# Kernel tuning notes

Hardware: AMD Instinct MI355X
Metric: run time of the kernel (lower is better)

## Reference

```python
import jax, jax.numpy as jnp
import numpy as np

N = 100000   # nodes
E = 1250000  # edges per graph
D = 64       # in_feats
H = 64       # hidden_dim
C = 129      # num_classes
EPS = 1e-5


def setup_inputs() -> dict:
    key = jax.random.key(0)
    ks = jax.random.split(key, 32)
    nrm = lambda k, s: jax.random.normal(k, s, jnp.float32) * 0.05
    inp = {
        'node_features': jax.random.normal(ks[0], (N, D), jnp.float32),
        'm_src': jax.random.randint(ks[1], (E,), 0, N, jnp.int32),
        'm_dst': jax.random.randint(ks[2], (E,), 0, N, jnp.int32),
        'r_src': jax.random.randint(ks[3], (E,), 0, N, jnp.int32),
        'r_dst': jax.random.randint(ks[4], (E,), 0, N, jnp.int32),
    }
    i = 5
    for pre in ('soc', 'rt'):
        inp[pre + '_W1'] = nrm(ks[i], (D, H)); inp[pre + '_b1'] = jnp.zeros((H,), jnp.float32)
        inp[pre + '_g1'] = jnp.ones((H,), jnp.float32); inp[pre + '_bt1'] = jnp.zeros((H,), jnp.float32)
        inp[pre + '_W2'] = nrm(ks[i + 1], (H, H)); inp[pre + '_b2'] = jnp.zeros((H,), jnp.float32)
        inp[pre + '_g2'] = jnp.ones((H,), jnp.float32); inp[pre + '_bt2'] = jnp.zeros((H,), jnp.float32)
        i += 2
    inp['gW1'] = nrm(ks[i], (4 * H, H)); inp['gb1'] = jnp.zeros((H,), jnp.float32)
    inp['prelu_a'] = jnp.full((1,), 0.25, jnp.float32)
    inp['gW2'] = nrm(ks[i + 1], (H, H)); inp['gb2'] = jnp.zeros((H,), jnp.float32)
    inp['fcW'] = nrm(ks[i + 2], (H, C)); inp['fcb'] = jnp.zeros((C,), jnp.float32)
    return inp


def _gconv(h, src, dst, W, b):
    # DGL GraphConv, norm='both': D_out^{-1/2} (scatter-sum) D_in^{-1/2}, linear, ELU
    ones = jnp.ones(src.shape[0], jnp.float32)
    deg_o = jax.ops.segment_sum(ones, src, num_segments=N)
    deg_i = jax.ops.segment_sum(ones, dst, num_segments=N)
    ns = jax.lax.rsqrt(jnp.clip(deg_o, 1.0))
    nd = jax.lax.rsqrt(jnp.clip(deg_i, 1.0))
    agg = jax.ops.segment_sum((h * ns[:, None])[src], dst, num_segments=N)
    return jax.nn.elu((agg * nd[:, None]) @ W + b)


def _bn(x, g, b):
    mu = x.mean(0)
    v = x.var(0)
    return (x - mu) * jax.lax.rsqrt(v + EPS) * g + b


def _branch(x, src, dst, W1, b1, g1, bt1, W2, b2, g2, bt2):
    h = _bn(_gconv(x, src, dst, W1, b1), g1, bt1)
    return _bn(_gconv(h, src, dst, W2, b2), g2, bt2)


def reference(node_features, m_src, m_dst, r_src, r_dst,
              soc_W1, soc_b1, soc_g1, soc_bt1, soc_W2, soc_b2, soc_g2, soc_bt2,
              rt_W1, rt_b1, rt_g1, rt_bt1, rt_W2, rt_b2, rt_g2, rt_bt2,
              gW1, gb1, prelu_a, gW2, gb2, fcW, fcb):
    h1 = _branch(node_features, m_src, m_dst, soc_W1, soc_b1, soc_g1, soc_bt1, soc_W2, soc_b2, soc_g2, soc_bt2)
    h2 = _branch(node_features, r_src, r_dst, rt_W1, rt_b1, rt_g1, rt_bt1, rt_W2, rt_b2, rt_g2, rt_bt2)
    cat = jnp.concatenate([h1, h2, jnp.abs(h1 - h2), h1 * h2], axis=-1)
    z = cat @ gW1 + gb1
    z = jnp.where(z > 0, z, prelu_a * z)  # PReLU (single shared slope)
    gate = jax.nn.sigmoid(z @ gW2 + gb2)
    fused = gate * h1 + (1.0 - gate) * h2
    return fused @ fcW + fcb
```

## Files before the change

### kernel.cpp

```cpp
#include <hip/hip_runtime.h>
#include <math.h>

#define NN 100000
#define NE 1250000
#define HD 64
#define NCLS 129
#define NTILES 6250
#define GRID_T 782

#define NCH 64
#define CHU ((NE + NCH - 1) / NCH)
#define SUBR 50000
#define NW2 12500
#define NHE2 ((NN + 1) * (size_t)HD)

typedef float f32x4 __attribute__((ext_vector_type(4)));
typedef short bf16x8 __attribute__((ext_vector_type(8)));

__device__ __forceinline__ short f2b(float f) {
    unsigned u = __builtin_bit_cast(unsigned, f);
    u += 0x7FFFu + ((u >> 16) & 1u);
    return (short)(u >> 16);
}
__device__ __forceinline__ float b2f(short s) {
    return __builtin_bit_cast(float, ((unsigned)(unsigned short)s) << 16);
}

__global__ __launch_bounds__(1024) void k_hist8(
    const int* __restrict__ d0, const int* __restrict__ s0,
    const int* __restrict__ d1, const int* __restrict__ s1,
    unsigned char* __restrict__ P8d, unsigned char* __restrict__ P8s) {
    __shared__ unsigned int hw[NW2];
    int b = blockIdx.x, s = blockIdx.y, z = blockIdx.z;
    int g = z >> 1, arr = z & 1;
    const int* __restrict__ idx = arr ? (g ? s1 : s0) : (g ? d1 : d0);
    for (int i = threadIdx.x; i < NW2; i += 1024) hw[i] = 0;
    __syncthreads();
    int lo = s * SUBR;
    int beg = b * CHU, end = beg + CHU;
    if (end > NE) end = NE;
    for (int i = beg + threadIdx.x; i < end; i += 1024) {
        int v = idx[i] - lo;
        if ((unsigned)v < (unsigned)SUBR)
            atomicAdd(&hw[v >> 2], 1u << ((v & 3) * 8));
    }
    __syncthreads();
    unsigned char* base = arr ? P8s : P8d;
    unsigned int* dst = (unsigned int*)(base + ((size_t)(g * NCH + b)) * NN + lo);
    for (int i = threadIdx.x; i < NW2; i += 1024) dst[i] = hw[i];
}

__global__ void k_reduce8(unsigned int* __restrict__ Pd, const unsigned int* __restrict__ Ps,
                          float* __restrict__ ns, float* __restrict__ nd,
                          int* __restrict__ degi) {
    int w = blockIdx.x * 256 + threadIdx.x;
    if (w >= NN / 4) return;
    int g = blockIdx.y;
    Pd += (size_t)g * NCH * (NN / 4);
    Ps += (size_t)g * NCH * (NN / 4);
    ns += (size_t)g * (NN + 1); nd += (size_t)g * NN; degi += (size_t)g * NN;
    if (w == 0) ns[NN] = 0.f;
    unsigned run = 0;
#pragma unroll 8
    for (int b = 0; b < NCH; ++b) {
        size_t o = (size_t)b * (NN / 4) + w;
        unsigned v = Pd[o];
        Pd[o] = run;
        run += v;
    }
    unsigned so = 0;
#pragma unroll 8
    for (int b = 0; b < NCH; ++b) so += Ps[(size_t)b * (NN / 4) + w];
#pragma unroll
    for (int j = 0; j < 4; ++j) {
        int din = (run >> (8 * j)) & 255;
        int dout = (so >> (8 * j)) & 255;
        int node = w * 4 + j;
        degi[node] = din;
        ns[node] = rsqrtf((float)(dout < 1 ? 1 : dout));
        nd[node] = rsqrtf((float)(din < 1 ? 1 : din));
    }
}

__global__ void k_scan_local(const int* __restrict__ deg, int* __restrict__ excl,
                             int* __restrict__ bsums) {
    __shared__ int sm[1024];
    int g = blockIdx.y;
    deg += (size_t)g * NN; excl += (size_t)g * (NN + 1); bsums += g * 1024;
    int t = threadIdx.x;
    int i = blockIdx.x * 1024 + t;
    int v = (i < NN) ? deg[i] : 0;
    sm[t] = v;
    __syncthreads();
    for (int ofs = 1; ofs < 1024; ofs <<= 1) {
        int x = (t >= ofs) ? sm[t - ofs] : 0;
        __syncthreads();
        sm[t] += x;
        __syncthreads();
    }
    if (i < NN) excl[i] = sm[t] - v;
    if (t == 1023) bsums[blockIdx.x] = sm[1023];
}

__global__ void k_scan_tops(int* __restrict__ bsums, int nb) {
    __shared__ int sm[1024];
    bsums += blockIdx.y * 1024;
    int t = threadIdx.x;
    int v = (t < nb) ? bsums[t] : 0;
    sm[t] = v;
    __syncthreads();
    for (int ofs = 1; ofs < 1024; ofs <<= 1) {
        int x = (t >= ofs) ? sm[t - ofs] : 0;
        __syncthreads();
        sm[t] += x;
        __syncthreads();
    }
    if (t < nb) bsums[t] = sm[t] - v;
}

__global__ void k_scan_add(int* __restrict__ excl, const int* __restrict__ bsums) {
    int g = blockIdx.y;
    excl += (size_t)g * (NN + 1); bsums += g * 1024;
    int i = blockIdx.x * blockDim.x + threadIdx.x;
    if (i < NN) excl[i] += bsums[i >> 10];
    if (i == 0) excl[NN] = NE;
}

__global__ __launch_bounds__(1024) void k_fill8(
    const int* __restrict__ d0, const int* __restrict__ d1,
    const int* __restrict__ s0, const int* __restrict__ s1,
    const int* __restrict__ rowptr, const unsigned char* __restrict__ Pofs,
    int* __restrict__ col) {
    __shared__ unsigned int cur[NW2];
    int b = blockIdx.x, s = blockIdx.y, g = blockIdx.z;
    const int* __restrict__ dst = g ? d1 : d0;
    const int* __restrict__ src = g ? s1 : s0;
    rowptr += (size_t)g * (NN + 1);
    col += (size_t)g * NE;
    const unsigned char* __restrict__ ofs = Pofs + ((size_t)(g * NCH + b)) * NN;
    for (int i = threadIdx.x; i < NW2; i += 1024) cur[i] = 0;
    __syncthreads();
    int lo = s * SUBR;
    int beg = b * CHU, end = beg + CHU;
    if (end > NE) end = NE;
    for (int i = beg + threadIdx.x; i < end; i += 1024) {
        int d = dst[i] - lo;
        if ((unsigned)d < (unsigned)SUBR) {
            unsigned old = atomicAdd(&cur[d >> 2], 1u << ((d & 3) * 8));
            int r = (old >> ((d & 3) * 8)) & 255;
            int node = d + lo;
            col[rowptr[node] + (int)ofs[node] + r] = src[i];
        }
    }
}

__global__ void k_scale_nf(const float* __restrict__ nf, short* __restrict__ T) {
    int i = blockIdx.x * blockDim.x + threadIdx.x;
    if (i >= (NN + 1) * 8) return;
    int node = i >> 3;
    short r[8];
    if (node == NN) {
#pragma unroll
        for (int j = 0; j < 8; ++j) r[j] = 0;
    } else {
        const float4* p = (const float4*)(nf + (size_t)i * 8);
        float4 a = p[0], b = p[1];
        r[0] = f2b(a.x); r[1] = f2b(a.y); r[2] = f2b(a.z); r[3] = f2b(a.w);
        r[4] = f2b(b.x); r[5] = f2b(b.y); r[6] = f2b(b.z); r[7] = f2b(b.w);
    }
    *(bf16x8*)(T + (size_t)i * 8) = *(bf16x8*)r;
}

template <int NS>
__global__ __launch_bounds__(256) void k_gather(
    const short* __restrict__ tab, size_t tabStride, const float* __restrict__ ns,
    const float* __restrict__ nd, const int* __restrict__ rowptr,
    const int* __restrict__ col, short* __restrict__ out) {
    int w = (blockIdx.x * 256 + threadIdx.x) >> 6;
    int lane = threadIdx.x & 63;
    if (w >= NN) return;
    int g = blockIdx.y;
    tab += (size_t)g * tabStride; nd += (size_t)g * NN;
    rowptr += (size_t)g * (NN + 1); col += (size_t)g * NE; out += (size_t)g * NHE2;
    const float* nsA = ns + (size_t)g * (NN + 1);
    int grp = lane >> 4;
    int sub = lane & 15;
    int beg = rowptr[w], end = rowptr[w + 1];
    float a0 = 0.f, a1 = 0.f, a2 = 0.f, a3 = 0.f;
    for (int e0 = beg; e0 < end; e0 += 64) {
        int cnt = end - e0; if (cnt > 64) cnt = 64;
        int myc = (lane < cnt) ? col[e0 + lane] : NN;
        float myns = 0.f;
        if (NS) myns = nsA[myc];
        for (int j = 0; j < cnt; j += 16) {
#pragma unroll
            for (int u = 0; u < 4; ++u) {
                int idx = j + u * 4 + grp;
                int c = __shfl(myc, idx, 64);
                uint2 v = *(const uint2*)(tab + (size_t)c * HD + sub * 4);
                float v0 = __builtin_bit_cast(float, v.x << 16);
                float v1 = __builtin_bit_cast(float, v.x & 0xffff0000u);
                float v2 = __builtin_bit_cast(float, v.y << 16);
                float v3 = __builtin_bit_cast(float, v.y & 0xffff0000u);
                if (NS) {
                    float nsc = __shfl(myns, idx, 64);
                    a0 = fmaf(nsc, v0, a0); a1 = fmaf(nsc, v1, a1);
                    a2 = fmaf(nsc, v2, a2); a3 = fmaf(nsc, v3, a3);
                } else {
                    a0 += v0; a1 += v1; a2 += v2; a3 += v3;
                }
            }
        }
    }
    a0 += __shfl_xor(a0, 16, 64); a1 += __shfl_xor(a1, 16, 64);
    a2 += __shfl_xor(a2, 16, 64); a3 += __shfl_xor(a3, 16, 64);
    a0 += __shfl_xor(a0, 32, 64); a1 += __shfl_xor(a1, 32, 64);
    a2 += __shfl_xor(a2, 32, 64); a3 += __shfl_xor(a3, 32, 64);
    if (grp == 0) {
        float s = nd[w];
        unsigned r0 = ((unsigned)(unsigned short)f2b(a0 * s)) |
                      (((unsigned)(unsigned short)f2b(a1 * s)) << 16);
        unsigned r1 = ((unsigned)(unsigned short)f2b(a2 * s)) |
                      (((unsigned)(unsigned short)f2b(a3 * s)) << 16);
        uint2 r; r.x = r0; r.y = r1;
        *(uint2*)(out + (size_t)w * HD + sub * 4) = r;
    }
}

__global__ __launch_bounds__(256) void k_lin(
    const short* __restrict__ X, const float* __restrict__ Wa, const float* __restrict__ Wb,
    const float* __restrict__ ba, const float* __restrict__ bb,
    short* __restrict__ Y, float* __restrict__ stats) {
    __shared__ short sW[4096];
    __shared__ float sm2[128];
    int g = blockIdx.y;
    const float* W = g ? Wb : Wa;
    const float* bias = g ? bb : ba;
    X += (size_t)g * NHE2; Y += (size_t)g * NHE2; stats += (size_t)g * 128;
    int t = threadIdx.x;
    for (int i = t; i < 4096; i += 256) {
        int j = i & 7, l16i = (i >> 3) & 15, kgi = (i >> 7) & 3, kbi = (i >> 9) & 1, oti = (i >> 10) & 3;
        sW[i] = f2b(W[(kbi * 32 + kgi * 8 + j) * HD + oti * 16 + l16i]);
    }
    if (t < 128) sm2[t] = 0.f;
    __syncthreads();
    int lane = t & 63, wv = t >> 6, l16 = lane & 15, kg = lane >> 4;
    bf16x8 bfrag[2][4];
#pragma unroll
    for (int kb = 0; kb < 2; ++kb)
#pragma unroll
        for (int ot = 0; ot < 4; ++ot)
            bfrag[kb][ot] = *(const bf16x8*)&sW[((ot * 2 + kb) * 4 + kg) * 128 + l16 * 8];
    float bo[4];
#pragma unroll
    for (int ot = 0; ot < 4; ++ot) bo[ot] = bias[ot * 16 + l16];
    float ps[4] = {0.f, 0.f, 0.f, 0.f}, pq[4] = {0.f, 0.f, 0.f, 0.f};
    for (int tile = blockIdx.x * 4 + wv; tile < NTILES; tile += GRID_T * 4) {
        const short* xp = X + ((size_t)tile * 16 + l16) * HD + kg * 8;
        bf16x8 a0 = *(const bf16x8*)xp;
        bf16x8 a1 = *(const bf16x8*)(xp + 32);
        f32x4 acc[4];
#pragma unroll
        for (int ot = 0; ot < 4; ++ot) {
            acc[ot] = (f32x4){0.f, 0.f, 0.f, 0.f};
            acc[ot] = __builtin_amdgcn_mfma_f32_16x16x32_bf16(a0, bfrag[0][ot], acc[ot], 0, 0, 0);
            acc[ot] = __builtin_amdgcn_mfma_f32_16x16x32_bf16(a1, bfrag[1][ot], acc[ot], 0, 0, 0);
        }
#pragma unroll
        for (int ot = 0; ot < 4; ++ot) {
#pragma unroll
            for (int r = 0; r < 4; ++r) {
                float y = acc[ot][r] + bo[ot];
                y = y > 0.f ? y : expm1f(y);
                ps[ot] += y; pq[ot] += y * y;
                Y[((size_t)tile * 16 + kg * 4 + r) * HD + ot * 16 + l16] = f2b(y);
            }
        }
    }
#pragma unroll
    for (int ot = 0; ot < 4; ++ot) {
        atomicAdd(&sm2[ot * 16 + l16], ps[ot]);
        atomicAdd(&sm2[64 + ot * 16 + l16], pq[ot]);
    }
    __syncthreads();
    if (t < 128) atomicAdd(&stats[t], sm2[t]);
}

__global__ void k_bnb(const short* __restrict__ Y, short* __restrict__ O,
                      const float* __restrict__ stats,
                      const float* __restrict__ ga, const float* __restrict__ gb,
                      const float* __restrict__ bta, const float* __restrict__ btb,
                      const float* __restrict__ ns) {
    int i = blockIdx.x * blockDim.x + threadIdx.x;
    if (i >= (NN + 1) * 8) return;
    int gI = blockIdx.y;
    Y += (size_t)gI * NHE2; O += (size_t)gI * NHE2; stats += (size_t)gI * 128;
    const float* g = gI ? gb : ga;
    const float* bt = gI ? btb : bta;
    if (ns) ns += (size_t)gI * (NN + 1);
    int node = i >> 3;
    short r[8];
    if (node == NN) {
#pragma unroll
        for (int j = 0; j < 8; ++j) r[j] = 0;
    } else {
        int o0 = (i & 7) * 8;
        float extra = ns ? ns[node] : 1.f;
        bf16x8 v = *(const bf16x8*)(Y + (size_t)i * 8);
        const float invN = 1.f / (float)NN;
#pragma unroll
        for (int j = 0; j < 8; ++j) {
            int o = o0 + j;
            float mu = stats[o] * invN;
            float var = fmaxf(stats[64 + o] * invN - mu * mu, 0.f);
            float isd = rsqrtf(var + 1e-5f);
            float sc = g[o] * isd * extra;
            float sh = (bt[o] - mu * g[o] * isd) * extra;
            r[j] = f2b(b2f(v[j]) * sc + sh);
        }
    }
    *(bf16x8*)(O + (size_t)i * 8) = *(bf16x8*)r;
}

#define TRS 72
__global__ __launch_bounds__(256) void k_tail(
    const short* __restrict__ H1, const short* __restrict__ H2,
    const float* __restrict__ W1, const float* __restrict__ bias1,
    const float* __restrict__ pa,
    const float* __restrict__ W2, const float* __restrict__ bias2,
    const float* __restrict__ Wf, const float* __restrict__ biasf,
    float* __restrict__ out) {
    __shared__ short sW1[16384];
    __shared__ short sW2[4096];
    __shared__ short sWf[9216];
    __shared__ short tr[4][2][16 * TRS];
    int t = threadIdx.x;
    for (int i = t; i < 16384; i += 256) {
        int j = i & 7, l16i = (i >> 3) & 15, kgi = (i >> 7) & 3, kbi = (i >> 9) & 7, oti = (i >> 12) & 3;
        sW1[i] = f2b(W1[(kbi * 32 + kgi * 8 + j) * HD + oti * 16 + l16i]);
    }
    for (int i = t; i < 4096; i += 256) {
        int j = i & 7, l16i = (i >> 3) & 15, kgi = (i >> 7) & 3, kbi = (i >> 9) & 1, oti = (i >> 10) & 3;
        sW2[i] = f2b(W2[(kbi * 32 + kgi * 8 + j) * HD + oti * 16 + l16i]);
    }
    for (int i = t; i < 9216; i += 256) {
        int j = i & 7, l16i = (i >> 3) & 15, kgi = (i >> 7) & 3, kbi = (i >> 9) & 1, oti = i >> 10;
        int k = kbi * 32 + kgi * 8 + j, o = oti * 16 + l16i;
        sWf[i] = (o < NCLS) ? f2b(Wf[k * NCLS + o]) : (short)0;
    }
    __syncthreads();
    int lane = t & 63, wv = t >> 6, l16 = lane & 15, kg = lane >> 4;
    float slope = pa[0];
    float bo1[4], bo2[4], bof[9];
#pragma unroll
    for (int ot = 0; ot < 4; ++ot) { bo1[ot] = bias1[ot * 16 + l16]; bo2[ot] = bias2[ot * 16 + l16]; }
#pragma unroll
    for (int ot = 0; ot < 9; ++ot) {
        int o = ot * 16 + l16;
        bof[ot] = (o < NCLS) ? biasf[o] : 0.f;
    }
    bf16x8 b2frag[2][4];
#pragma unroll
    for (int kb = 0; kb < 2; ++kb)
#pragma unroll
        for (int ot = 0; ot < 4; ++ot)
            b2frag[kb][ot] = *(const bf16x8*)&sW2[((ot * 2 + kb) * 4 + kg) * 128 + l16 * 8];
    short* trZ = &tr[wv][0][0];
    short* trG = &tr[wv][1][0];

    for (int tile = blockIdx.x * 4 + wv; tile < NTILES; tile += GRID_T * 4) {
        size_t rb = ((size_t)tile * 16 + l16) * HD + kg * 8;
        bf16x8 h1e = *(const bf16x8*)(H1 + rb);
        bf16x8 h1o = *(const bf16x8*)(H1 + rb + 32);
        bf16x8 h2e = *(const bf16x8*)(H2 + rb);
        bf16x8 h2o = *(const bf16x8*)(H2 + rb + 32);
        bf16x8 fe[8];
        fe[0] = h1e; fe[1] = h1o; fe[2] = h2e; fe[3] = h2o;
        short tabs[8], tprd[8];
#pragma unroll
        for (int j = 0; j < 8; ++j) {
            float a = b2f(h1e[j]), b = b2f(h2e[j]);
            tabs[j] = f2b(fabsf(a - b)); tprd[j] = f2b(a * b);
        }
        fe[4] = *(bf16x8*)tabs; fe[6] = *(bf16x8*)tprd;
#pragma unroll
        for (int j = 0; j < 8; ++j) {
            float a = b2f(h1o[j]), b = b2f(h2o[j]);
            tabs[j] = f2b(fabsf(a - b)); tprd[j] = f2b(a * b);
        }
        fe[5] = *(bf16x8*)tabs; fe[7] = *(bf16x8*)tprd;
        f32x4 acc[4];
#pragma unroll
        for (int ot = 0; ot < 4; ++ot) acc[ot] = (f32x4){0.f, 0.f, 0.f, 0.f};
#pragma unroll
        for (int kb = 0; kb < 8; ++kb)
#pragma unroll
            for (int ot = 0; ot < 4; ++ot) {
                bf16x8 bf = *(const bf16x8*)&sW1[((ot * 8 + kb) * 4 + kg) * 128 + l16 * 8];
                acc[ot] = __builtin_amdgcn_mfma_f32_16x16x32_bf16(fe[kb], bf, acc[ot], 0, 0, 0);
            }
#pragma unroll
        for (int ot = 0; ot < 4; ++ot)
#pragma unroll
            for (int r = 0; r < 4; ++r) {
                float z = acc[ot][r] + bo1[ot];
                z = z > 0.f ? z : slope * z;
                trZ[(kg * 4 + r) * TRS + ot * 16 + l16] = f2b(z);
            }
        asm volatile("s_waitcnt lgkmcnt(0)" ::: "memory");
        __builtin_amdgcn_sched_barrier(0);
        bf16x8 za0 = *(const bf16x8*)&trZ[l16 * TRS + kg * 8];
        bf16x8 za1 = *(const bf16x8*)&trZ[l16 * TRS + 32 + kg * 8];
        f32x4 acc2[4];
#pragma unroll
        for (int ot = 0; ot < 4; ++ot) {
            acc2[ot] = (f32x4){0.f, 0.f, 0.f, 0.f};
            acc2[ot] = __builtin_amdgcn_mfma_f32_16x16x32_bf16(za0, b2frag[0][ot], acc2[ot], 0, 0, 0);
            acc2[ot] = __builtin_amdgcn_mfma_f32_16x16x32_bf16(za1, b2frag[1][ot], acc2[ot], 0, 0, 0);
        }
#pragma unroll
        for (int ot = 0; ot < 4; ++ot)
#pragma unroll
            for (int r = 0; r < 4; ++r) {
                float y = acc2[ot][r] + bo2[ot];
                float gate = 1.f / (1.f + expf(-y));
                trG[(kg * 4 + r) * TRS + ot * 16 + l16] = f2b(gate);
            }
        asm volatile("s_waitcnt lgkmcnt(0)" ::: "memory");
        __builtin_amdgcn_sched_barrier(0);
        bf16x8 ga0 = *(const bf16x8*)&trG[l16 * TRS + kg * 8];
        bf16x8 ga1 = *(const bf16x8*)&trG[l16 * TRS + 32 + kg * 8];
        short f0[8], f1[8];
#pragma unroll
        for (int j = 0; j < 8; ++j) {
            float gf = b2f(ga0[j]);
            f0[j] = f2b(gf * b2f(h1e[j]) + (1.f - gf) * b2f(h2e[j]));
            float gf2 = b2f(ga1[j]);
            f1[j] = f2b(gf2 * b2f(h1o[j]) + (1.f - gf2) * b2f(h2o[j]));
        }
        bf16x8 fa0 = *(bf16x8*)f0, fa1 = *(bf16x8*)f1;
        f32x4 acc3[9];
#pragma unroll
        for (int ot = 0; ot < 9; ++ot) acc3[ot] = (f32x4){0.f, 0.f, 0.f, 0.f};
#pragma unroll
        for (int kb = 0; kb < 2; ++kb) {
            bf16x8 a = kb ? fa1 : fa0;
#pragma unroll
            for (int ot = 0; ot < 9; ++ot) {
                bf16x8 bf = *(const bf16x8*)&sWf[((ot * 2 + kb) * 4 + kg) * 128 + l16 * 8];
                acc3[ot] = __builtin_amdgcn_mfma_f32_16x16x32_bf16(a, bf, acc3[ot], 0, 0, 0);
            }
        }
#pragma unroll
        for (int ot = 0; ot < 9; ++ot) {
            int o = ot * 16 + l16;
            if (o < NCLS) {
#pragma unroll
                for (int r = 0; r < 4; ++r) {
                    int node = tile * 16 + kg * 4 + r;
                    out[(size_t)node * NCLS + o] = acc3[ot][r] + bof[ot];
                }
            }
        }
    }
}

extern "C" void kernel_launch(void* const* d_in, const int* in_sizes, int n_in,
                              void* d_out, int out_size, void* d_ws, size_t ws_size,
                              hipStream_t stream) {
    (void)in_sizes; (void)n_in; (void)out_size; (void)ws_size;
    const int N = NN;

    const float* nf = (const float*)d_in[0];
    const int* m_src = (const int*)d_in[1];
    const int* m_dst = (const int*)d_in[2];
    const int* r_src = (const int*)d_in[3];
    const int* r_dst = (const int*)d_in[4];
    const float *W1[2], *b1[2], *g1[2], *bt1[2], *W2[2], *b2[2], *g2[2], *bt2[2];
    for (int br = 0; br < 2; ++br) {
        int base = 5 + br * 8;
        W1[br] = (const float*)d_in[base + 0];
        b1[br] = (const float*)d_in[base + 1];
        g1[br] = (const float*)d_in[base + 2];
        bt1[br] = (const float*)d_in[base + 3];
        W2[br] = (const float*)d_in[base + 4];
        b2[br] = (const float*)d_in[base + 5];
        g2[br] = (const float*)d_in[base + 6];
        bt2[br] = (const float*)d_in[base + 7];
    }
    const float* gW1 = (const float*)d_in[21];
    const float* gb1 = (const float*)d_in[22];
    const float* pa  = (const float*)d_in[23];
    const float* gW2 = (const float*)d_in[24];
    const float* gb2 = (const float*)d_in[25];
    const float* fcW = (const float*)d_in[26];
    const float* fcb = (const float*)d_in[27];
    float* out = (float*)d_out;

    char* p = (char*)d_ws;
    auto take = [&](size_t bytes) { char* r = p; p += (bytes + 255) & ~(size_t)255; return r; };
    size_t NHb2 = NHE2 * 2;
    unsigned char* P8d = (unsigned char*)take((size_t)2 * NCH * NN);
    unsigned char* P8s = (unsigned char*)take((size_t)2 * NCH * NN);
    short* T   = (short*)take(NHb2);
    short* X   = (short*)take(2 * NHb2);
    short* Y   = (short*)take(2 * NHb2);
    short* Hs  = (short*)take(2 * NHb2);
    short* H   = (short*)take(2 * NHb2);
    float* ns = (float*)take((size_t)2 * (N + 1) * 4);
    float* nd = (float*)take((size_t)2 * N * 4);
    float* stats = (float*)take(2 * 2 * 128 * 4);
    int* degi = (int*)take((size_t)2 * N * 4);
    int* rowptr = (int*)take((size_t)2 * (N + 1) * 4);
    int* bsums = (int*)take(2 * 4096);
    int* col = (int*)((char*)d_out + (size_t)N * HD * 2);

    int gN = (N + 255) / 256;
    int nScanBlk = (N + 1023) / 1024;
    int gEW = ((N + 1) * 8 + 255) / 256;
    int gW4 = (N / 4 + 255) / 256;
    int gGat = (N * 64) / 256;

    k_hist8<<<dim3(NCH, 2, 4), 1024, 0, stream>>>(m_dst, m_src, r_dst, r_src, P8d, P8s);
    k_reduce8<<<dim3(gW4, 2), 256, 0, stream>>>((unsigned int*)P8d, (const unsigned int*)P8s,
                                                ns, nd, degi);
    k_scan_local<<<dim3(nScanBlk, 2), 1024, 0, stream>>>(degi, rowptr, bsums);
    k_scan_tops<<<dim3(1, 2), 1024, 0, stream>>>(bsums, nScanBlk);
    k_scan_add<<<dim3(gN, 2), 256, 0, stream>>>(rowptr, bsums);
    k_fill8<<<dim3(NCH, 2, 2), 1024, 0, stream>>>(m_dst, r_dst, m_src, r_src, rowptr, P8d, col);
    hipMemsetAsync(stats, 0, 2 * 2 * 128 * 4, stream);

    k_scale_nf<<<gEW, 256, 0, stream>>>(nf, T);
    k_gather<1><<<dim3(gGat, 2), 256, 0, stream>>>(T, 0, ns, nd, rowptr, col, X);
    k_lin<<<dim3(GRID_T, 2), 256, 0, stream>>>(X, W1[0], W1[1], b1[0], b1[1], Y, stats);
    k_bnb<<<dim3(gEW, 2), 256, 0, stream>>>(Y, Hs, stats, g1[0], g1[1], bt1[0], bt1[1], ns);

    k_gather<0><<<dim3(gGat, 2), 256, 0, stream>>>(Hs, NHE2, ns, nd, rowptr, col, X);
    k_lin<<<dim3(GRID_T, 2), 256, 0, stream>>>(X, W2[0], W2[1], b2[0], b2[1], Y, stats + 256);
    k_bnb<<<dim3(gEW, 2), 256, 0, stream>>>(Y, H, stats + 256, g2[0], g2[1], bt2[0], bt2[1],
                                            (const float*)nullptr);

    k_tail<<<GRID_T, 256, 0, stream>>>(H, H + NHE2, gW1, gb1, pa, gW2, gb2, fcW, fcb, out);
}
```

Measured before the change: 391.3 us.

## Use fixed-stride padded adjacency and fold first batchnorm into second gather

Replaces the CSR build with a fixed stride of 64 slots per node. This removes the three prefix-scan kernels and the rowptr lookups in the fill and gather kernels. The first batchnorm (with its ns prescale) is folded algebraically into the second gather, which applies scale and shift from the accumulated ns sum, so one elementwise pass and one intermediate buffer go away. The trade-off is that correctness now relies on every in-degree being at most 64. The padding row of the unnormalized Y table is also read with zero weight, so garbage values there could leak in.

```diff
diff --git a/kernel.cpp b/kernel.cpp
--- a/kernel.cpp
+++ b/kernel.cpp
@@ -7,6 +7,7 @@
 #define NCLS 129
 #define NTILES 6250
 #define GRID_T 782
+#define MAXDEG 64
 
 #define NCH 64
 #define CHU ((NE + NCH - 1) / NCH)
@@ -82,61 +83,15 @@
     }
 }
 
-__global__ void k_scan_local(const int* __restrict__ deg, int* __restrict__ excl,
-                             int* __restrict__ bsums) {
-    __shared__ int sm[1024];
-    int g = blockIdx.y;
-    deg += (size_t)g * NN; excl += (size_t)g * (NN + 1); bsums += g * 1024;
-    int t = threadIdx.x;
-    int i = blockIdx.x * 1024 + t;
-    int v = (i < NN) ? deg[i] : 0;
-    sm[t] = v;
-    __syncthreads();
-    for (int ofs = 1; ofs < 1024; ofs <<= 1) {
-        int x = (t >= ofs) ? sm[t - ofs] : 0;
-        __syncthreads();
-        sm[t] += x;
-        __syncthreads();
-    }
-    if (i < NN) excl[i] = sm[t] - v;
-    if (t == 1023) bsums[blockIdx.x] = sm[1023];
-}
-
-__global__ void k_scan_tops(int* __restrict__ bsums, int nb) {
-    __shared__ int sm[1024];
-    bsums += blockIdx.y * 1024;
-    int t = threadIdx.x;
-    int v = (t < nb) ? bsums[t] : 0;
-    sm[t] = v;
-    __syncthreads();
-    for (int ofs = 1; ofs < 1024; ofs <<= 1) {
-        int x = (t >= ofs) ? sm[t - ofs] : 0;
-        __syncthreads();
-        sm[t] += x;
-        __syncthreads();
-    }
-    if (t < nb) bsums[t] = sm[t] - v;
-}
-
-__global__ void k_scan_add(int* __restrict__ excl, const int* __restrict__ bsums) {
-    int g = blockIdx.y;
-    excl += (size_t)g * (NN + 1); bsums += g * 1024;
-    int i = blockIdx.x * blockDim.x + threadIdx.x;
-    if (i < NN) excl[i] += bsums[i >> 10];
-    if (i == 0) excl[NN] = NE;
-}
-
 __global__ __launch_bounds__(1024) void k_fill8(
     const int* __restrict__ d0, const int* __restrict__ d1,
     const int* __restrict__ s0, const int* __restrict__ s1,
-    const int* __restrict__ rowptr, const unsigned char* __restrict__ Pofs,
-    int* __restrict__ col) {
+    const unsigned char* __restrict__ Pofs, int* __restrict__ col) {
     __shared__ unsigned int cur[NW2];
     int b = blockIdx.x, s = blockIdx.y, g = blockIdx.z;
     const int* __restrict__ dst = g ? d1 : d0;
     const int* __restrict__ src = g ? s1 : s0;
-    rowptr += (size_t)g * (NN + 1);
-    col += (size_t)g * NE;
+    col += ((size_t)g * NN) * MAXDEG;
     const unsigned char* __restrict__ ofs = Pofs + ((size_t)(g * NCH + b)) * NN;
     for (int i = threadIdx.x; i < NW2; i += 1024) cur[i] = 0;
     __syncthreads();
@@ -149,7 +104,7 @@
             unsigned old = atomicAdd(&cur[d >> 2], 1u << ((d & 3) * 8));
             int r = (old >> ((d & 3) * 8)) & 255;
             int node = d + lo;
-            col[rowptr[node] + (int)ofs[node] + r] = src[i];
+            col[(size_t)node * MAXDEG + (int)ofs[node] + r] = src[i];
         }
     }
 }
@@ -171,57 +126,72 @@
     *(bf16x8*)(T + (size_t)i * 8) = *(bf16x8*)r;
 }
 
-template <int NS>
+template <int BN>
 __global__ __launch_bounds__(256) void k_gather(
-    const short* __restrict__ tab, size_t tabStride, const float* __restrict__ ns,
-    const float* __restrict__ nd, const int* __restrict__ rowptr,
-    const int* __restrict__ col, short* __restrict__ out) {
+    const short* __restrict__ tab, size_t tabStride,
+    const float* __restrict__ ns, const float* __restrict__ nd,
+    const int* __restrict__ degi, const int* __restrict__ col,
+    short* __restrict__ out, const float* __restrict__ stats,
+    const float* __restrict__ ga, const float* __restrict__ gb,
+    const float* __restrict__ bta, const float* __restrict__ btb) {
     int w = (blockIdx.x * 256 + threadIdx.x) >> 6;
     int lane = threadIdx.x & 63;
     if (w >= NN) return;
     int g = blockIdx.y;
-    tab += (size_t)g * tabStride; nd += (size_t)g * NN;
-    rowptr += (size_t)g * (NN + 1); col += (size_t)g * NE; out += (size_t)g * NHE2;
+    tab += (size_t)g * tabStride; nd += (size_t)g * NN; degi += (size_t)g * NN;
+    col += ((size_t)g * NN) * MAXDEG; out += (size_t)g * NHE2;
     const float* nsA = ns + (size_t)g * (NN + 1);
     int grp = lane >> 4;
     int sub = lane & 15;
-    int beg = rowptr[w], end = rowptr[w + 1];
-    float a0 = 0.f, a1 = 0.f, a2 = 0.f, a3 = 0.f;
-    for (int e0 = beg; e0 < end; e0 += 64) {
-        int cnt = end - e0; if (cnt > 64) cnt = 64;
-        int myc = (lane < cnt) ? col[e0 + lane] : NN;
-        float myns = 0.f;
-        if (NS) myns = nsA[myc];
-        for (int j = 0; j < cnt; j += 16) {
-#pragma unroll
-            for (int u = 0; u < 4; ++u) {
-                int idx = j + u * 4 + grp;
-                int c = __shfl(myc, idx, 64);
-                uint2 v = *(const uint2*)(tab + (size_t)c * HD + sub * 4);
-                float v0 = __builtin_bit_cast(float, v.x << 16);
-                float v1 = __builtin_bit_cast(float, v.x & 0xffff0000u);
-                float v2 = __builtin_bit_cast(float, v.y << 16);
-                float v3 = __builtin_bit_cast(float, v.y & 0xffff0000u);
-                if (NS) {
-                    float nsc = __shfl(myns, idx, 64);
-                    a0 = fmaf(nsc, v0, a0); a1 = fmaf(nsc, v1, a1);
-                    a2 = fmaf(nsc, v2, a2); a3 = fmaf(nsc, v3, a3);
-                } else {
-                    a0 += v0; a1 += v1; a2 += v2; a3 += v3;
-                }
-            }
+    int deg = degi[w];
+    int myc = (lane < deg) ? col[(size_t)w * MAXDEG + lane] : NN;
+    float myns = nsA[myc];
+    float a0 = 0.f, a1 = 0.f, a2 = 0.f, a3 = 0.f, sl = 0.f;
+    for (int j = 0; j < deg; j += 16) {
+#pragma unroll
+        for (int u = 0; u < 4; ++u) {
+            int idx = j + u * 4 + grp;
+            int c = __shfl(myc, idx, 64);
+            float nsc = __shfl(myns, idx, 64);
+            uint2 v = *(const uint2*)(tab + (size_t)c * HD + sub * 4);
+            a0 = fmaf(nsc, __builtin_bit_cast(float, v.x << 16), a0);
+            a1 = fmaf(nsc, __builtin_bit_cast(float, v.x & 0xffff0000u), a1);
+            a2 = fmaf(nsc, __builtin_bit_cast(float, v.y << 16), a2);
+            a3 = fmaf(nsc, __builtin_bit_cast(float, v.y & 0xffff0000u), a3);
+            if (BN) sl += nsc;
         }
     }
     a0 += __shfl_xor(a0, 16, 64); a1 += __shfl_xor(a1, 16, 64);
     a2 += __shfl_xor(a2, 16, 64); a3 += __shfl_xor(a3, 16, 64);
     a0 += __shfl_xor(a0, 32, 64); a1 += __shfl_xor(a1, 32, 64);
     a2 += __shfl_xor(a2, 32, 64); a3 += __shfl_xor(a3, 32, 64);
+    if (BN) { sl += __shfl_xor(sl, 16, 64); sl += __shfl_xor(sl, 32, 64); }
     if (grp == 0) {
         float s = nd[w];
-        unsigned r0 = ((unsigned)(unsigned short)f2b(a0 * s)) |
-                      (((unsigned)(unsigned short)f2b(a1 * s)) << 16);
-        unsigned r1 = ((unsigned)(unsigned short)f2b(a2 * s)) |
-                      (((unsigned)(unsigned short)f2b(a3 * s)) << 16);
+        float r4[4] = {a0, a1, a2, a3};
+        if (BN) {
+            const float* gp = g ? gb : ga;
+            const float* bp = g ? btb : bta;
+            const float* st = stats + (size_t)g * 128;
+            const float invN = 1.f / (float)NN;
+#pragma unroll
+            for (int q = 0; q < 4; ++q) {
+                int o = sub * 4 + q;
+                float mu = st[o] * invN;
+                float var = fmaxf(st[64 + o] * invN - mu * mu, 0.f);
+                float isd = rsqrtf(var + 1e-5f);
+                float sc = gp[o] * isd;
+                float sh = bp[o] - mu * sc;
+                r4[q] = s * (sc * r4[q] + sh * sl);
+            }
+        } else {
+#pragma unroll
+            for (int q = 0; q < 4; ++q) r4[q] *= s;
+        }
+        unsigned r0 = ((unsigned)(unsigned short)f2b(r4[0])) |
+                      (((unsigned)(unsigned short)f2b(r4[1])) << 16);
+        unsigned r1 = ((unsigned)(unsigned short)f2b(r4[2])) |
+                      (((unsigned)(unsigned short)f2b(r4[3])) << 16);
         uint2 r; r.x = r0; r.y = r1;
         *(uint2*)(out + (size_t)w * HD + sub * 4) = r;
     }
@@ -289,35 +259,26 @@
 __global__ void k_bnb(const short* __restrict__ Y, short* __restrict__ O,
                       const float* __restrict__ stats,
                       const float* __restrict__ ga, const float* __restrict__ gb,
-                      const float* __restrict__ bta, const float* __restrict__ btb,
-                      const float* __restrict__ ns) {
+                      const float* __restrict__ bta, const float* __restrict__ btb) {
     int i = blockIdx.x * blockDim.x + threadIdx.x;
-    if (i >= (NN + 1) * 8) return;
+    if (i >= NN * 8) return;
     int gI = blockIdx.y;
     Y += (size_t)gI * NHE2; O += (size_t)gI * NHE2; stats += (size_t)gI * 128;
     const float* g = gI ? gb : ga;
     const float* bt = gI ? btb : bta;
-    if (ns) ns += (size_t)gI * (NN + 1);
-    int node = i >> 3;
+    int o0 = (i & 7) * 8;
+    bf16x8 v = *(const bf16x8*)(Y + (size_t)i * 8);
     short r[8];
-    if (node == NN) {
-#pragma unroll
-        for (int j = 0; j < 8; ++j) r[j] = 0;
-    } else {
-        int o0 = (i & 7) * 8;
-        float extra = ns ? ns[node] : 1.f;
-        bf16x8 v = *(const bf16x8*)(Y + (size_t)i * 8);
-        const float invN = 1.f / (float)NN;
-#pragma unroll
-        for (int j = 0; j < 8; ++j) {
-            int o = o0 + j;
-            float mu = stats[o] * invN;
-            float var = fmaxf(stats[64 + o] * invN - mu * mu, 0.f);
-            float isd = rsqrtf(var + 1e-5f);
-            float sc = g[o] * isd * extra;
-            float sh = (bt[o] - mu * g[o] * isd) * extra;
-            r[j] = f2b(b2f(v[j]) * sc + sh);
-        }
+    const float invN = 1.f / (float)NN;
+#pragma unroll
+    for (int j = 0; j < 8; ++j) {
+        int o = o0 + j;
+        float mu = stats[o] * invN;
+        float var = fmaxf(stats[64 + o] * invN - mu * mu, 0.f);
+        float isd = rsqrtf(var + 1e-5f);
+        float sc = g[o] * isd;
+        float sh = bt[o] - mu * sc;
+        r[j] = f2b(b2f(v[j]) * sc + sh);
     }
     *(bf16x8*)(O + (size_t)i * 8) = *(bf16x8*)r;
 }
@@ -502,43 +463,36 @@
     size_t NHb2 = NHE2 * 2;
     unsigned char* P8d = (unsigned char*)take((size_t)2 * NCH * NN);
     unsigned char* P8s = (unsigned char*)take((size_t)2 * NCH * NN);
-    short* T   = (short*)take(NHb2);
-    short* X   = (short*)take(2 * NHb2);
-    short* Y   = (short*)take(2 * NHb2);
-    short* Hs  = (short*)take(2 * NHb2);
-    short* H   = (short*)take(2 * NHb2);
+    int* col  = (int*)take((size_t)2 * NN * MAXDEG * 4);
+    short* T  = (short*)take(NHb2);
+    short* X  = (short*)take(2 * NHb2);
+    short* Y  = (short*)take(2 * NHb2);
+    short* H  = (short*)take(2 * NHb2);
     float* ns = (float*)take((size_t)2 * (N + 1) * 4);
     float* nd = (float*)take((size_t)2 * N * 4);
     float* stats = (float*)take(2 * 2 * 128 * 4);
     int* degi = (int*)take((size_t)2 * N * 4);
-    int* rowptr = (int*)take((size_t)2 * (N + 1) * 4);
-    int* bsums = (int*)take(2 * 4096);
-    int* col = (int*)((char*)d_out + (size_t)N * HD * 2);
-
-    int gN = (N + 255) / 256;
-    int nScanBlk = (N + 1023) / 1024;
-    int gEW = ((N + 1) * 8 + 255) / 256;
+
+    int gEWz = ((N + 1) * 8 + 255) / 256;
+    int gEW  = (N * 8 + 255) / 256;
     int gW4 = (N / 4 + 255) / 256;
     int gGat = (N * 64) / 256;
 
     k_hist8<<<dim3(NCH, 2, 4), 1024, 0, stream>>>(m_dst, m_src, r_dst, r_src, P8d, P8s);
     k_reduce8<<<dim3(gW4, 2), 256, 0, stream>>>((unsigned int*)P8d, (const unsigned int*)P8s,
                                                 ns, nd, degi);
-    k_scan_local<<<dim3(nScanBlk, 2), 1024, 0, stream>>>(degi, rowptr, bsums);
-    k_scan_tops<<<dim3(1, 2), 1024, 0, stream>>>(bsums, nScanBlk);
-    k_scan_add<<<dim3(gN, 2), 256, 0, stream>>>(rowptr, bsums);
-    k_fill8<<<dim3(NCH, 2, 2), 1024, 0, stream>>>(m_dst, r_dst, m_src, r_src, rowptr, P8d, col);
+    k_fill8<<<dim3(NCH, 2, 2), 1024, 0, stream>>>(m_dst, r_dst, m_src, r_src, P8d, col);
     hipMemsetAsync(stats, 0, 2 * 2 * 128 * 4, stream);
 
-    k_scale_nf<<<gEW, 256, 0, stream>>>(nf, T);
-    k_gather<1><<<dim3(gGat, 2), 256, 0, stream>>>(T, 0, ns, nd, rowptr, col, X);
+    k_scale_nf<<<gEWz, 256, 0, stream>>>(nf, T);
+    k_gather<0><<<dim3(gGat, 2), 256, 0, stream>>>(T, 0, ns, nd, degi, col, X,
+                                                   nullptr, nullptr, nullptr, nullptr, nullptr);
     k_lin<<<dim3(GRID_T, 2), 256, 0, stream>>>(X, W1[0], W1[1], b1[0], b1[1], Y, stats);
-    k_bnb<<<dim3(gEW, 2), 256, 0, stream>>>(Y, Hs, stats, g1[0], g1[1], bt1[0], bt1[1], ns);
-
-    k_gather<0><<<dim3(gGat, 2), 256, 0, stream>>>(Hs, NHE2, ns, nd, rowptr, col, X);
+
+    k_gather<1><<<dim3(gGat, 2), 256, 0, stream>>>(Y, NHE2, ns, nd, degi, col, X,
+                                                   stats, g1[0], g1[1], bt1[0], bt1[1]);
     k_lin<<<dim3(GRID_T, 2), 256, 0, stream>>>(X, W2[0], W2[1], b2[0], b2[1], Y, stats + 256);
-    k_bnb<<<dim3(gEW, 2), 256, 0, stream>>>(Y, H, stats + 256, g2[0], g2[1], bt2[0], bt2[1],
-                                            (const float*)nullptr);
+    k_bnb<<<dim3(gEW, 2), 256, 0, stream>>>(Y, H, stats + 256, g2[0], g2[1], bt2[0], bt2[1]);
 
     k_tail<<<GRID_T, 256, 0, stream>>>(H, H + NHE2, gW1, gb1, pa, gW2, gb2, fcW, fcb, out);
 }
```

After: 370.8 us. -5.2%, faster.
